# Optimization experiments

Hardware: AMD Instinct MI355X
Metric: run time of the kernel (lower is better)

Reference implementation:

```python
import jax, jax.numpy as jnp
import numpy as np
from jax import lax

RHO = 1.0
LAMDA = 0.1
ADMM_ITERS = 10


def setup_inputs() -> dict:
    key = jax.random.key(0)
    k1, k2, k3, k4 = jax.random.split(key, 4)
    B, M, A, MULT = 2048, 512, 2048, 3
    S = A * MULT
    y = jax.random.normal(k1, (B, M), dtype=jnp.float32)
    x = jax.random.normal(k2, (B, A), dtype=jnp.float32)
    # measurement matrix buffer: randn(m, ambient)/sqrt(m)
    a = jax.random.normal(k3, (M, A), dtype=jnp.float32) / np.sqrt(M)
    # phi: kaiming_normal_ on (ambient*mult, ambient): std = sqrt(2/fan_in)
    phi = jax.random.normal(k4, (S, A), dtype=jnp.float32) * np.sqrt(2.0 / A)
    return {"y": y, "x": x, "a": a, "phi": phi}


def _shrink(v, thresh):
    return jnp.sign(v) * jnp.maximum(jnp.zeros_like(v), jnp.abs(v) - thresh)


def reference(y, x, a, phi):
    B = y.shape[0]
    x = x.reshape(B, -1)
    y = y.reshape(B, -1)
    min_x = jnp.min(x)
    max_x = jnp.max(x)
    S = phi.shape[0]
    u = jnp.zeros((B, S), dtype=y.dtype)
    z = jnp.zeros((B, S), dtype=y.dtype)

    # multiplier(rho): m = a^T a + rho * phi^T phi, LU-factor, invert L and U.
    m = a.T @ a + RHO * (phi.T @ phi)
    _, L, U = jax.scipy.linalg.lu(m)
    # NOTE: original uses einsum('aa,ba->ba', Linv, v) which contracts the
    # repeated index -> uses only diag(Linv) elementwise. Replicate exactly.
    dL = jnp.diagonal(jnp.linalg.inv(L))  # (A,) -- unit-lower -> ones
    dU = jnp.diagonal(jnp.linalg.inv(U))  # (A,)

    # x0 = einsum('am,bm->ba', a.T, y) = y @ a  -> (B, A)
    x0 = y @ a
    rho_phi = RHO * phi  # (S, A)

    def step(carry, _):
        u, z, _xh = carry
        # einsum('as,bs->ba', rho*phi.T, z-u) = (z-u) @ (rho*phi)
        x_L = dL * (x0 + (z - u) @ rho_phi)            # (B, A)
        x_hat = dU * x_L                                # (B, A)
        fxu = x_hat @ phi.T + u                         # (B, S)
        z_new = _shrink(fxu, LAMDA / RHO)
        u_new = u + fxu - z_new
        return (u_new, z_new, x_hat), None

    xh0 = jnp.zeros((B, x.shape[1]), dtype=y.dtype)
    (u, z, x_hat), _ = lax.scan(step, (u, z, xh0), None, length=ADMM_ITERS)
    return jnp.clip(x_hat, min_x, max_x)
```

## Files before the change

### kernel.cpp

```cpp
#include <hip/hip_runtime.h>

#define B_N 2048
#define M_N 512
#define A_N 2048
#define S_N 6144
#define SHRINK_T 0.1f
#define ADMM_ITERS 10

#define SPLIT_SCALE 512.0f
#define INV_SPLIT (1.0f / 512.0f)

typedef _Float16 v8h __attribute__((ext_vector_type(8)));
typedef _Float16 v4h __attribute__((ext_vector_type(4)));
typedef float v4f __attribute__((ext_vector_type(4)));

#define AS1 __attribute__((address_space(1)))
#define AS3 __attribute__((address_space(3)))

__device__ __forceinline__ float shrinkf(float v) {
  return copysignf(fmaxf(fabsf(v) - SHRINK_T, 0.f), v);
}

__device__ __forceinline__ void dma16(const _Float16* g, int ld, int r0, int k0,
                                      int slot, _Float16* region) {
  int m = slot >> 2;
  int k8 = (slot & 3) ^ ((m >> 1) & 3);
  const _Float16* gp = g + (size_t)(r0 + m) * ld + k0 + (k8 << 3);
  __builtin_amdgcn_global_load_lds((const AS1 void*)gp,
                                   (AS3 void*)(region + (size_t)(slot & ~63) * 8), 16, 0, 0);
}

template <int EPI>
__global__ __launch_bounds__(256, 2) void mgemm(
    const _Float16* __restrict__ Ah0, const _Float16* __restrict__ Al0, int ldA0, int K0,
    const _Float16* __restrict__ Bh0, const _Float16* __restrict__ Bl0, int ldB0,
    const _Float16* __restrict__ Ah1, const _Float16* __restrict__ Al1, int ldA1, int K1,
    const _Float16* __restrict__ Bh1, const _Float16* __restrict__ Bl1, int ldB1,
    float* __restrict__ C, int ldC, const float* __restrict__ dU,
    _Float16* __restrict__ Oh, _Float16* __restrict__ Ol, float* __restrict__ U) {
  __shared__ _Float16 lds[2 * 16384];
  const int tid = threadIdx.x;
  const int i0 = blockIdx.y * 128, j0 = blockIdx.x * 128;
  const int lane = tid & 63, w = tid >> 6, wm = w >> 1, wn = w & 1;
  const int fb = (lane & 15) * 32 + (((lane >> 4) ^ ((lane >> 1) & 3)) << 3);

  v4f acc1[4][4], acc2[4][4];
  const v4f z4 = {0.f, 0.f, 0.f, 0.f};
#pragma unroll
  for (int tm = 0; tm < 4; ++tm)
#pragma unroll
    for (int tn = 0; tn < 4; ++tn) { acc1[tm][tn] = z4; acc2[tm][tn] = z4; }

  const int steps0 = K0 >> 5, steps1 = K1 >> 5, total = steps0 + steps1;

  auto issue = [&](int s, _Float16* buf) {
    const _Float16 *Ah, *Al, *Bh, *Bl;
    int ldA, ldB, k0;
    if (s < steps0) {
      Ah = Ah0; Al = Al0; Bh = Bh0; Bl = Bl0; ldA = ldA0; ldB = ldB0; k0 = s << 5;
    } else {
      Ah = Ah1; Al = Al1; Bh = Bh1; Bl = Bl1; ldA = ldA1; ldB = ldB1; k0 = (s - steps0) << 5;
    }
    dma16(Ah, ldA, i0, k0, tid,       buf);
    dma16(Ah, ldA, i0, k0, 256 + tid, buf);
    dma16(Al, ldA, i0, k0, tid,       buf + 4096);
    dma16(Al, ldA, i0, k0, 256 + tid, buf + 4096);
    dma16(Bh, ldB, j0, k0, tid,       buf + 8192);
    dma16(Bh, ldB, j0, k0, 256 + tid, buf + 8192);
    dma16(Bl, ldB, j0, k0, tid,       buf + 12288);
    dma16(Bl, ldB, j0, k0, 256 + tid, buf + 12288);
  };

  issue(0, lds);
  int cur = 0;
  for (int s = 0; s < total; ++s) {
    __syncthreads();
    if (s + 1 < total) issue(s + 1, lds + (cur ^ 1) * 16384);
    const _Float16* L = lds + cur * 16384;
    v8h ah[4], al[4], bh[4], bl[4];
#pragma unroll
    for (int tm = 0; tm < 4; ++tm) {
      int off = (wm * 64 + tm * 16) * 32 + fb;
      ah[tm] = *(const v8h*)(L + off);
      al[tm] = *(const v8h*)(L + 4096 + off);
    }
#pragma unroll
    for (int tn = 0; tn < 4; ++tn) {
      int off = (wn * 64 + tn * 16) * 32 + fb;
      bh[tn] = *(const v8h*)(L + 8192 + off);
      bl[tn] = *(const v8h*)(L + 12288 + off);
    }
#pragma unroll
    for (int tm = 0; tm < 4; ++tm)
#pragma unroll
      for (int tn = 0; tn < 4; ++tn) {
        acc1[tm][tn] = __builtin_amdgcn_mfma_f32_16x16x32_f16(ah[tm], bh[tn], acc1[tm][tn], 0, 0, 0);
        v4f c2 = acc2[tm][tn];
        c2 = __builtin_amdgcn_mfma_f32_16x16x32_f16(ah[tm], bl[tn], c2, 0, 0, 0);
        c2 = __builtin_amdgcn_mfma_f32_16x16x32_f16(al[tm], bh[tn], c2, 0, 0, 0);
        acc2[tm][tn] = c2;
      }
    cur ^= 1;
  }

  const int q = lane >> 4, lr = lane & 15;
#pragma unroll
  for (int tm = 0; tm < 4; ++tm)
#pragma unroll
    for (int tn = 0; tn < 4; ++tn) {
      int row0 = i0 + wm * 64 + tm * 16 + q * 4;
      int col = j0 + wn * 64 + tn * 16 + lr;
      if constexpr (EPI == 0) {
#pragma unroll
        for (int r = 0; r < 4; ++r) {
          size_t o = (size_t)(row0 + r) * ldC + col;
          C[o] = acc1[tm][tn][r] + acc2[tm][tn][r] * INV_SPLIT;
        }
      } else if constexpr (EPI == 1) {
        float du = dU[col];
#pragma unroll
        for (int r = 0; r < 4; ++r) {
          size_t o = (size_t)(row0 + r) * ldC + col;
          float v = (acc1[tm][tn][r] + acc2[tm][tn][r] * INV_SPLIT) * du;
          C[o] = v;
          _Float16 h = (_Float16)v;
          Oh[o] = h;
          Ol[o] = (_Float16)((v - (float)h) * SPLIT_SCALE);
        }
      } else {
#pragma unroll
        for (int r = 0; r < 4; ++r) {
          size_t o = (size_t)(row0 + r) * ldC + col;
          float uo = U[o];
          float fx = acc1[tm][tn][r] + acc2[tm][tn][r] * INV_SPLIT + uo;
          float zn = shrinkf(fx);
          float un = uo + fx - zn;
          U[o] = un;
          float zu = zn - un;
          _Float16 h = (_Float16)zu;
          Oh[o] = h;
          Ol[o] = (_Float16)((zu - (float)h) * SPLIT_SCALE);
        }
      }
    }
}

__global__ __launch_bounds__(256) void split_kernel(const float* __restrict__ s,
                                                    _Float16* __restrict__ h,
                                                    _Float16* __restrict__ l, int n4) {
  for (int i = blockIdx.x * 256 + threadIdx.x; i < n4; i += gridDim.x * 256) {
    float4 v = ((const float4*)s)[i];
    v4h hh, ll;
    hh.x = (_Float16)v.x; ll.x = (_Float16)((v.x - (float)hh.x) * SPLIT_SCALE);
    hh.y = (_Float16)v.y; ll.y = (_Float16)((v.y - (float)hh.y) * SPLIT_SCALE);
    hh.z = (_Float16)v.z; ll.z = (_Float16)((v.z - (float)hh.z) * SPLIT_SCALE);
    hh.w = (_Float16)v.w; ll.w = (_Float16)((v.w - (float)hh.w) * SPLIT_SCALE);
    ((v4h*)h)[i] = hh;
    ((v4h*)l)[i] = ll;
  }
}

__global__ __launch_bounds__(256) void tsplit_kernel(const float* __restrict__ src, int R, int C,
                                                     _Float16* __restrict__ h,
                                                     _Float16* __restrict__ l) {
  __shared__ float t[32][33];
  int br = blockIdx.y * 32, bc = blockIdx.x * 32;
  int r = threadIdx.x >> 3, c4 = (threadIdx.x & 7) * 4;
  float4 v = *(const float4*)(src + (size_t)(br + r) * C + bc + c4);
  t[r][c4 + 0] = v.x; t[r][c4 + 1] = v.y; t[r][c4 + 2] = v.z; t[r][c4 + 3] = v.w;
  __syncthreads();
  int a = threadIdx.x >> 3, r4 = (threadIdx.x & 7) * 4;
  float x0 = t[r4 + 0][a], x1 = t[r4 + 1][a], x2 = t[r4 + 2][a], x3 = t[r4 + 3][a];
  v4h hh, ll;
  hh.x = (_Float16)x0; ll.x = (_Float16)((x0 - (float)hh.x) * SPLIT_SCALE);
  hh.y = (_Float16)x1; ll.y = (_Float16)((x1 - (float)hh.y) * SPLIT_SCALE);
  hh.z = (_Float16)x2; ll.z = (_Float16)((x2 - (float)hh.z) * SPLIT_SCALE);
  hh.w = (_Float16)x3; ll.w = (_Float16)((x3 - (float)hh.w) * SPLIT_SCALE);
  size_t o = (size_t)(bc + a) * R + br + r4;
  *(v4h*)(h + o) = hh;
  *(v4h*)(l + o) = ll;
}

__global__ __launch_bounds__(256) void chol64_kernel(float* __restrict__ mm,
                                                     float* __restrict__ dU, int kb) {
  __shared__ float Ad[64][65];
  int tid = threadIdx.x;
  for (int e = tid; e < 64 * 64; e += 256) {
    int r = e >> 6, c = e & 63;
    Ad[r][c] = mm[(size_t)(kb + r) * A_N + kb + c];
  }
  __syncthreads();
  for (int j = 0; j < 64; ++j) {
    if (tid == 0) Ad[j][j] = sqrtf(Ad[j][j]);
    __syncthreads();
    if (tid > j && tid < 64) Ad[tid][j] /= Ad[j][j];
    __syncthreads();
    int i = j + 1 + (tid >> 2);
    int q = tid & 3;
    if (i < 64) {
      float lij = Ad[i][j];
      for (int t = j + 1 + q; t <= i; t += 4)
        Ad[i][t] = fmaf(-lij, Ad[t][j], Ad[i][t]);
    }
    __syncthreads();
  }
  if (tid < 64) {
    float d = Ad[tid][tid];
    dU[kb + tid] = 1.0f / (d * d);
  }
  for (int e = tid; e < 64 * 64; e += 256) {
    int r = e >> 6, c = e & 63;
    if (c <= r) mm[(size_t)(kb + r) * A_N + kb + c] = Ad[r][c];
  }
}

__global__ __launch_bounds__(256) void trsm64_kernel(float* __restrict__ mm, int kb) {
  __shared__ float Ls[64][65];
  int tid = threadIdx.x;
  for (int e = tid; e < 64 * 64; e += 256) {
    int r = e >> 6, c = e & 63;
    Ls[r][c] = mm[(size_t)(kb + r) * A_N + kb + c];
  }
  __syncthreads();
  int row = kb + 64 + blockIdx.x * 256 + tid;
  if (row >= A_N) return;
  float v[64];
  float* gr = mm + (size_t)row * A_N + kb;
#pragma unroll
  for (int qq = 0; qq < 16; ++qq) {
    float4 t = *(const float4*)(gr + qq * 4);
    v[qq * 4 + 0] = t.x; v[qq * 4 + 1] = t.y;
    v[qq * 4 + 2] = t.z; v[qq * 4 + 3] = t.w;
  }
#pragma unroll
  for (int j = 0; j < 64; ++j) {
    float s = v[j];
#pragma unroll
    for (int t = 0; t < j; ++t) s = fmaf(-v[t], Ls[j][t], s);
    v[j] = s / Ls[j][j];
  }
#pragma unroll
  for (int qq = 0; qq < 16; ++qq)
    *(float4*)(gr + qq * 4) =
        make_float4(v[qq * 4 + 0], v[qq * 4 + 1], v[qq * 4 + 2], v[qq * 4 + 3]);
}

__global__ __launch_bounds__(256) void syrk64_kernel(float* __restrict__ mm, int kb) {
  __shared__ float As[16 * 64];
  __shared__ float Bs[16 * 64];
  int tid = threadIdx.x, tx = tid & 15, ty = tid >> 4;
  int base = kb + 64;
  int i0 = base + blockIdx.y * 64;
  int j0 = base + blockIdx.x * 64;
  float acc[4][4] = {{0.f}};
  for (int k0 = 0; k0 < 64; k0 += 16) {
    __syncthreads();
    {
      int ii = tid >> 2, k4 = (tid & 3) * 4;
      float4 vv = *(const float4*)(mm + (size_t)(i0 + ii) * A_N + kb + k0 + k4);
      As[(k4 + 0) * 64 + ii] = vv.x; As[(k4 + 1) * 64 + ii] = vv.y;
      As[(k4 + 2) * 64 + ii] = vv.z; As[(k4 + 3) * 64 + ii] = vv.w;
      float4 ww = *(const float4*)(mm + (size_t)(j0 + ii) * A_N + kb + k0 + k4);
      Bs[(k4 + 0) * 64 + ii] = ww.x; Bs[(k4 + 1) * 64 + ii] = ww.y;
      Bs[(k4 + 2) * 64 + ii] = ww.z; Bs[(k4 + 3) * 64 + ii] = ww.w;
    }
    __syncthreads();
#pragma unroll
    for (int k = 0; k < 16; ++k) {
      float4 a0 = *(const float4*)(As + k * 64 + ty * 4);
      float4 b0 = *(const float4*)(Bs + k * 64 + tx * 4);
      float av[4] = {a0.x, a0.y, a0.z, a0.w};
      float bv[4] = {b0.x, b0.y, b0.z, b0.w};
#pragma unroll
      for (int i = 0; i < 4; ++i)
#pragma unroll
        for (int j = 0; j < 4; ++j) acc[i][j] = fmaf(av[i], bv[j], acc[i][j]);
    }
  }
#pragma unroll
  for (int i = 0; i < 4; ++i) {
    float* p = mm + (size_t)(i0 + ty * 4 + i) * A_N + j0 + tx * 4;
    float4 c = *(const float4*)p;
    c.x -= acc[i][0]; c.y -= acc[i][1]; c.z -= acc[i][2]; c.w -= acc[i][3];
    *(float4*)p = c;
  }
}

__device__ __forceinline__ unsigned fkey(float v) {
  unsigned b = __float_as_uint(v);
  return (b & 0x80000000u) ? ~b : (b | 0x80000000u);
}
__device__ __forceinline__ float key2f(unsigned k) {
  unsigned b = (k & 0x80000000u) ? (k & 0x7FFFFFFFu) : ~k;
  return __uint_as_float(b);
}

__global__ void minmax_init(unsigned* keys) {
  keys[0] = 0xFFFFFFFFu;
  keys[1] = 0u;
}

__global__ __launch_bounds__(256) void minmax_kernel(const float* __restrict__ x,
                                                     unsigned* __restrict__ keys, int n4) {
  unsigned mn = 0xFFFFFFFFu, mx = 0u;
  for (int i = blockIdx.x * 256 + threadIdx.x; i < n4; i += gridDim.x * 256) {
    float4 v = ((const float4*)x)[i];
    unsigned k0 = fkey(v.x), k1 = fkey(v.y), k2 = fkey(v.z), k3 = fkey(v.w);
    mn = min(mn, min(min(k0, k1), min(k2, k3)));
    mx = max(mx, max(max(k0, k1), max(k2, k3)));
  }
  for (int o = 32; o > 0; o >>= 1) {
    mn = min(mn, (unsigned)__shfl_down((int)mn, o));
    mx = max(mx, (unsigned)__shfl_down((int)mx, o));
  }
  if ((threadIdx.x & 63) == 0) {
    atomicMin(&keys[0], mn);
    atomicMax(&keys[1], mx);
  }
}

__global__ __launch_bounds__(256) void clip_kernel(const float* __restrict__ xh,
                                                   const unsigned* __restrict__ keys,
                                                   float* __restrict__ out, int n4) {
  float mn = key2f(keys[0]);
  float mx = key2f(keys[1]);
  for (int i = blockIdx.x * 256 + threadIdx.x; i < n4; i += gridDim.x * 256) {
    float4 v = ((const float4*)xh)[i];
    v.x = fminf(fmaxf(v.x, mn), mx);
    v.y = fminf(fmaxf(v.y, mn), mx);
    v.z = fminf(fmaxf(v.z, mn), mx);
    v.w = fminf(fmaxf(v.w, mn), mx);
    ((float4*)out)[i] = v;
  }
}

extern "C" void kernel_launch(void* const* d_in, const int* in_sizes, int n_in,
                              void* d_out, int out_size, void* d_ws, size_t ws_size,
                              hipStream_t stream) {
  const float* y   = (const float*)d_in[0];
  const float* x   = (const float*)d_in[1];
  const float* a   = (const float*)d_in[2];
  const float* phi = (const float*)d_in[3];
  float* out = (float*)d_out;

  char* ws = (char*)d_ws;
  size_t off = 0;
  auto alloc = [&](size_t bytes) -> void* {
    void* p = ws + off;
    off = (off + bytes + 255) & ~(size_t)255;
    return p;
  };
  float* mm = (float*)alloc(sizeof(float) * (size_t)A_N * A_N);
  float* u  = (float*)alloc(sizeof(float) * (size_t)B_N * S_N);
  float* dU = (float*)alloc(sizeof(float) * A_N);
  unsigned* keys = (unsigned*)alloc(sizeof(unsigned) * 2);
  _Float16* phi_h  = (_Float16*)alloc(2 * (size_t)S_N * A_N);
  _Float16* phi_l  = (_Float16*)alloc(2 * (size_t)S_N * A_N);
  _Float16* phiT_h = (_Float16*)alloc(2 * (size_t)A_N * S_N);
  _Float16* phiT_l = (_Float16*)alloc(2 * (size_t)A_N * S_N);
  _Float16* aT_h   = (_Float16*)alloc(2 * (size_t)A_N * M_N);
  _Float16* aT_l   = (_Float16*)alloc(2 * (size_t)A_N * M_N);
  _Float16* y_h    = (_Float16*)alloc(2 * (size_t)B_N * M_N);
  _Float16* y_l    = (_Float16*)alloc(2 * (size_t)B_N * M_N);
  _Float16* zu_h   = (_Float16*)alloc(2 * (size_t)B_N * S_N);
  _Float16* zu_l   = (_Float16*)alloc(2 * (size_t)B_N * S_N);
  _Float16* xh_h   = (_Float16*)alloc(2 * (size_t)B_N * A_N);
  _Float16* xh_l   = (_Float16*)alloc(2 * (size_t)B_N * A_N);
  float* xh32 = mm;

  minmax_init<<<1, 1, 0, stream>>>(keys);
  minmax_kernel<<<1024, 256, 0, stream>>>(x, keys, (B_N * A_N) / 4);

  split_kernel<<<2048, 256, 0, stream>>>(phi, phi_h, phi_l, (S_N * A_N) / 4);
  split_kernel<<<512, 256, 0, stream>>>(y, y_h, y_l, (B_N * M_N) / 4);
  tsplit_kernel<<<dim3(A_N / 32, S_N / 32), 256, 0, stream>>>(phi, S_N, A_N, phiT_h, phiT_l);
  tsplit_kernel<<<dim3(A_N / 32, M_N / 32), 256, 0, stream>>>(a, M_N, A_N, aT_h, aT_l);

  mgemm<0><<<dim3(A_N / 128, A_N / 128), 256, 0, stream>>>(
      aT_h, aT_l, M_N, M_N, aT_h, aT_l, M_N,
      phiT_h, phiT_l, S_N, S_N, phiT_h, phiT_l, S_N,
      mm, A_N, nullptr, nullptr, nullptr, nullptr);

  for (int kb = 0; kb < A_N; kb += 64) {
    chol64_kernel<<<1, 256, 0, stream>>>(mm, dU, kb);
    int rows = A_N - kb - 64;
    if (rows > 0) {
      trsm64_kernel<<<(rows + 255) / 256, 256, 0, stream>>>(mm, kb);
      syrk64_kernel<<<dim3(rows / 64, rows / 64), 256, 0, stream>>>(mm, kb);
    }
  }

  hipMemsetAsync(u, 0, sizeof(float) * (size_t)B_N * S_N, stream);
  hipMemsetAsync(zu_h, 0, 2 * (size_t)B_N * S_N, stream);
  hipMemsetAsync(zu_l, 0, 2 * (size_t)B_N * S_N, stream);

  for (int it = 0; it < ADMM_ITERS; ++it) {
    mgemm<1><<<dim3(A_N / 128, B_N / 128), 256, 0, stream>>>(
        zu_h, zu_l, S_N, S_N, phiT_h, phiT_l, S_N,
        y_h, y_l, M_N, M_N, aT_h, aT_l, M_N,
        xh32, A_N, dU, xh_h, xh_l, nullptr);
    if (it < ADMM_ITERS - 1) {
      mgemm<2><<<dim3(S_N / 128, B_N / 128), 256, 0, stream>>>(
          xh_h, xh_l, A_N, A_N, phi_h, phi_l, A_N,
          nullptr, nullptr, 0, 0, nullptr, nullptr, 0,
          nullptr, S_N, nullptr, zu_h, zu_l, u);
    }
  }

  clip_kernel<<<1024, 256, 0, stream>>>(xh32, keys, out, (B_N * A_N) / 4);
}
```

Before: 6.892 ms.

## Deepen GEMM prefetch, skip zero first iteration, fuse clip into final GEMM

The GEMM main loop now keeps two tile loads in flight, using waitcnt on outstanding vector-memory ops plus split barriers instead of one syncthreads per step. The first ADMM iteration skips the z-u GEMM contribution (K=0) and the first update kernel treats u as zero, so the memsets of u and zu are removed. The fp32 x_hat store is dropped from intermediate iterations, and the clip is fused into a new epilogue of the last GEMM, which removes the separate clip kernel. The hand-written waitcnt encodings and barrier placement must match the hardware's counters exactly, or tiles could be read before they land.

```diff
diff --git a/kernel.cpp b/kernel.cpp
--- a/kernel.cpp
+++ b/kernel.cpp
@@ -17,8 +17,20 @@
 #define AS1 __attribute__((address_space(1)))
 #define AS3 __attribute__((address_space(3)))
 
+#define WAITCNT_VM8 0xF78
+#define WAITCNT_VM0 0xF70
+
 __device__ __forceinline__ float shrinkf(float v) {
   return copysignf(fmaxf(fabsf(v) - SHRINK_T, 0.f), v);
+}
+
+__device__ __forceinline__ unsigned fkey(float v) {
+  unsigned b = __float_as_uint(v);
+  return (b & 0x80000000u) ? ~b : (b | 0x80000000u);
+}
+__device__ __forceinline__ float key2f(unsigned k) {
+  unsigned b = (k & 0x80000000u) ? (k & 0x7FFFFFFFu) : ~k;
+  return __uint_as_float(b);
 }
 
 __device__ __forceinline__ void dma16(const _Float16* g, int ld, int r0, int k0,
@@ -30,14 +42,15 @@
                                    (AS3 void*)(region + (size_t)(slot & ~63) * 8), 16, 0, 0);
 }
 
-template <int EPI>
+template <int EPI, bool FZ>
 __global__ __launch_bounds__(256, 2) void mgemm(
     const _Float16* __restrict__ Ah0, const _Float16* __restrict__ Al0, int ldA0, int K0,
     const _Float16* __restrict__ Bh0, const _Float16* __restrict__ Bl0, int ldB0,
     const _Float16* __restrict__ Ah1, const _Float16* __restrict__ Al1, int ldA1, int K1,
     const _Float16* __restrict__ Bh1, const _Float16* __restrict__ Bl1, int ldB1,
     float* __restrict__ C, int ldC, const float* __restrict__ dU,
-    _Float16* __restrict__ Oh, _Float16* __restrict__ Ol, float* __restrict__ U) {
+    _Float16* __restrict__ Oh, _Float16* __restrict__ Ol, float* __restrict__ U,
+    const unsigned* __restrict__ kk) {
   __shared__ _Float16 lds[2 * 16384];
   const int tid = threadIdx.x;
   const int i0 = blockIdx.y * 128, j0 = blockIdx.x * 128;
@@ -72,11 +85,16 @@
   };
 
   issue(0, lds);
-  int cur = 0;
+  if (total > 1) issue(1, lds + 16384);
+
   for (int s = 0; s < total; ++s) {
-    __syncthreads();
-    if (s + 1 < total) issue(s + 1, lds + (cur ^ 1) * 16384);
-    const _Float16* L = lds + cur * 16384;
+    if (s + 1 < total) __builtin_amdgcn_s_waitcnt(WAITCNT_VM8);
+    else               __builtin_amdgcn_s_waitcnt(WAITCNT_VM0);
+    __asm__ volatile("" ::: "memory");
+    __builtin_amdgcn_s_barrier();
+    __asm__ volatile("" ::: "memory");
+
+    const _Float16* L = lds + (s & 1) * 16384;
     v8h ah[4], al[4], bh[4], bl[4];
 #pragma unroll
     for (int tm = 0; tm < 4; ++tm) {
@@ -100,10 +118,18 @@
         c2 = __builtin_amdgcn_mfma_f32_16x16x32_f16(al[tm], bh[tn], c2, 0, 0, 0);
         acc2[tm][tn] = c2;
       }
-    cur ^= 1;
+
+    if (s + 2 < total) {
+      __asm__ volatile("" ::: "memory");
+      __builtin_amdgcn_s_barrier();
+      __asm__ volatile("" ::: "memory");
+      issue(s + 2, lds + (s & 1) * 16384);
+    }
   }
 
   const int q = lane >> 4, lr = lane & 15;
+  float mn = 0.f, mx = 0.f;
+  if constexpr (EPI == 3) { mn = key2f(kk[0]); mx = key2f(kk[1]); }
 #pragma unroll
   for (int tm = 0; tm < 4; ++tm)
 #pragma unroll
@@ -122,16 +148,23 @@
         for (int r = 0; r < 4; ++r) {
           size_t o = (size_t)(row0 + r) * ldC + col;
           float v = (acc1[tm][tn][r] + acc2[tm][tn][r] * INV_SPLIT) * du;
-          C[o] = v;
           _Float16 h = (_Float16)v;
           Oh[o] = h;
           Ol[o] = (_Float16)((v - (float)h) * SPLIT_SCALE);
         }
-      } else {
+      } else if constexpr (EPI == 3) {
+        float du = dU[col];
 #pragma unroll
         for (int r = 0; r < 4; ++r) {
           size_t o = (size_t)(row0 + r) * ldC + col;
-          float uo = U[o];
+          float v = (acc1[tm][tn][r] + acc2[tm][tn][r] * INV_SPLIT) * du;
+          C[o] = fminf(fmaxf(v, mn), mx);
+        }
+      } else {
+#pragma unroll
+        for (int r = 0; r < 4; ++r) {
+          size_t o = (size_t)(row0 + r) * ldC + col;
+          float uo = FZ ? 0.f : U[o];
           float fx = acc1[tm][tn][r] + acc2[tm][tn][r] * INV_SPLIT + uo;
           float zn = shrinkf(fx);
           float un = uo + fx - zn;
@@ -286,15 +319,6 @@
   }
 }
 
-__device__ __forceinline__ unsigned fkey(float v) {
-  unsigned b = __float_as_uint(v);
-  return (b & 0x80000000u) ? ~b : (b | 0x80000000u);
-}
-__device__ __forceinline__ float key2f(unsigned k) {
-  unsigned b = (k & 0x80000000u) ? (k & 0x7FFFFFFFu) : ~k;
-  return __uint_as_float(b);
-}
-
 __global__ void minmax_init(unsigned* keys) {
   keys[0] = 0xFFFFFFFFu;
   keys[1] = 0u;
@@ -316,21 +340,6 @@
   if ((threadIdx.x & 63) == 0) {
     atomicMin(&keys[0], mn);
     atomicMax(&keys[1], mx);
-  }
-}
-
-__global__ __launch_bounds__(256) void clip_kernel(const float* __restrict__ xh,
-                                                   const unsigned* __restrict__ keys,
-                                                   float* __restrict__ out, int n4) {
-  float mn = key2f(keys[0]);
-  float mx = key2f(keys[1]);
-  for (int i = blockIdx.x * 256 + threadIdx.x; i < n4; i += gridDim.x * 256) {
-    float4 v = ((const float4*)xh)[i];
-    v.x = fminf(fmaxf(v.x, mn), mx);
-    v.y = fminf(fmaxf(v.y, mn), mx);
-    v.z = fminf(fmaxf(v.z, mn), mx);
-    v.w = fminf(fmaxf(v.w, mn), mx);
-    ((float4*)out)[i] = v;
   }
 }
 
@@ -366,7 +375,6 @@
   _Float16* zu_l   = (_Float16*)alloc(2 * (size_t)B_N * S_N);
   _Float16* xh_h   = (_Float16*)alloc(2 * (size_t)B_N * A_N);
   _Float16* xh_l   = (_Float16*)alloc(2 * (size_t)B_N * A_N);
-  float* xh32 = mm;
 
   minmax_init<<<1, 1, 0, stream>>>(keys);
   minmax_kernel<<<1024, 256, 0, stream>>>(x, keys, (B_N * A_N) / 4);
@@ -376,10 +384,10 @@
   tsplit_kernel<<<dim3(A_N / 32, S_N / 32), 256, 0, stream>>>(phi, S_N, A_N, phiT_h, phiT_l);
   tsplit_kernel<<<dim3(A_N / 32, M_N / 32), 256, 0, stream>>>(a, M_N, A_N, aT_h, aT_l);
 
-  mgemm<0><<<dim3(A_N / 128, A_N / 128), 256, 0, stream>>>(
+  mgemm<0, false><<<dim3(A_N / 128, A_N / 128), 256, 0, stream>>>(
       aT_h, aT_l, M_N, M_N, aT_h, aT_l, M_N,
       phiT_h, phiT_l, S_N, S_N, phiT_h, phiT_l, S_N,
-      mm, A_N, nullptr, nullptr, nullptr, nullptr);
+      mm, A_N, nullptr, nullptr, nullptr, nullptr, nullptr);
 
   for (int kb = 0; kb < A_N; kb += 64) {
     chol64_kernel<<<1, 256, 0, stream>>>(mm, dU, kb);
@@ -390,22 +398,30 @@
     }
   }
 
-  hipMemsetAsync(u, 0, sizeof(float) * (size_t)B_N * S_N, stream);
-  hipMemsetAsync(zu_h, 0, 2 * (size_t)B_N * S_N, stream);
-  hipMemsetAsync(zu_l, 0, 2 * (size_t)B_N * S_N, stream);
-
   for (int it = 0; it < ADMM_ITERS; ++it) {
-    mgemm<1><<<dim3(A_N / 128, B_N / 128), 256, 0, stream>>>(
-        zu_h, zu_l, S_N, S_N, phiT_h, phiT_l, S_N,
-        y_h, y_l, M_N, M_N, aT_h, aT_l, M_N,
-        xh32, A_N, dU, xh_h, xh_l, nullptr);
+    int Kzu = (it == 0) ? 0 : S_N;
     if (it < ADMM_ITERS - 1) {
-      mgemm<2><<<dim3(S_N / 128, B_N / 128), 256, 0, stream>>>(
-          xh_h, xh_l, A_N, A_N, phi_h, phi_l, A_N,
-          nullptr, nullptr, 0, 0, nullptr, nullptr, 0,
-          nullptr, S_N, nullptr, zu_h, zu_l, u);
-    }
-  }
-
-  clip_kernel<<<1024, 256, 0, stream>>>(xh32, keys, out, (B_N * A_N) / 4);
-}
+      mgemm<1, false><<<dim3(A_N / 128, B_N / 128), 256, 0, stream>>>(
+          zu_h, zu_l, S_N, Kzu, phiT_h, phiT_l, S_N,
+          y_h, y_l, M_N, M_N, aT_h, aT_l, M_N,
+          nullptr, A_N, dU, xh_h, xh_l, nullptr, nullptr);
+    } else {
+      mgemm<3, false><<<dim3(A_N / 128, B_N / 128), 256, 0, stream>>>(
+          zu_h, zu_l, S_N, Kzu, phiT_h, phiT_l, S_N,
+          y_h, y_l, M_N, M_N, aT_h, aT_l, M_N,
+          out, A_N, dU, nullptr, nullptr, nullptr, keys);
+    }
+    if (it < ADMM_ITERS - 1) {
+      if (it == 0)
+        mgemm<2, true><<<dim3(S_N / 128, B_N / 128), 256, 0, stream>>>(
+            xh_h, xh_l, A_N, A_N, phi_h, phi_l, A_N,
+            nullptr, nullptr, 0, 0, nullptr, nullptr, 0,
+            nullptr, S_N, nullptr, zu_h, zu_l, u, nullptr);
+      else
+        mgemm<2, false><<<dim3(S_N / 128, B_N / 128), 256, 0, stream>>>(
+            xh_h, xh_l, A_N, A_N, phi_h, phi_l, A_N,
+            nullptr, nullptr, 0, 0, nullptr, nullptr, 0,
+            nullptr, S_N, nullptr, zu_h, zu_l, u, nullptr);
+    }
+  }
+}
```

New measurement: 6.503 ms. 5.6% less time.
